# Kernel tuning notes

Measured on AMD Instinct MI355X. Metric: run time of the kernel, lower is better.

## Reference

```python
import math
import jax, jax.numpy as jnp
import numpy as np

B, T, D = 2, 2048, 1024
NUM_HEADS = 16
NUM_KV_HEADS = 4
HEAD_DIM = 64
ROPE_THETA = 500000.0


def precompute_freqs_cis(dim, seq_len, theta):
    freqs = 1.0 / theta ** (jnp.arange(0, dim, 2).astype(jnp.float32) / dim)
    freqs = jnp.outer(jnp.arange(seq_len), freqs)  # [T, dim//2]
    return jnp.cos(freqs), jnp.sin(freqs)


def apply_rotary_emb(xq, xk, cos, sin):
    # xq:[B,T,H,Dh], cos/sin:[T,Dh//2] -> broadcast as [1,T,1,Dh//2]
    c = cos[None, :, None, :]
    s = sin[None, :, None, :]

    def rot(x):
        xr = x.reshape(*x.shape[:-1], -1, 2)
        x0, x1 = xr[..., 0], xr[..., 1]
        return jnp.stack([x0 * c - x1 * s, x1 * c + x0 * s], axis=-1).reshape(x.shape)

    return rot(xq), rot(xk)


def setup_inputs() -> dict:
    key = jax.random.key(0)
    ks = jax.random.split(key, 5)
    x = jax.random.normal(ks[0], (B, T, D), dtype=jnp.float32)
    # causal mask [B,1,T,T]
    mask = jnp.broadcast_to(jnp.tril(jnp.ones((T, T), dtype=bool))[None, None], (B, 1, T, T))
    sq = 1.0 / math.sqrt(D)
    Wq = jax.random.normal(ks[1], (D, NUM_HEADS * HEAD_DIM), dtype=jnp.float32) * sq
    Wk = jax.random.normal(ks[2], (D, NUM_KV_HEADS * HEAD_DIM), dtype=jnp.float32) * sq
    Wv = jax.random.normal(ks[3], (D, NUM_KV_HEADS * HEAD_DIM), dtype=jnp.float32) * sq
    Wo = jax.random.normal(ks[4], (NUM_HEADS * HEAD_DIM, D), dtype=jnp.float32) * (1.0 / math.sqrt(NUM_HEADS * HEAD_DIM))
    return {"x": x, "mask": mask, "Wq": Wq, "Wk": Wk, "Wv": Wv, "Wo": Wo}


def reference(x, mask, Wq, Wk, Wv, Wo):
    b, t, _ = x.shape
    n_rep = NUM_HEADS // NUM_KV_HEADS
    q = (x @ Wq).reshape(b, t, NUM_HEADS, HEAD_DIM)
    k = (x @ Wk).reshape(b, t, NUM_KV_HEADS, HEAD_DIM)
    v = (x @ Wv).reshape(b, t, NUM_KV_HEADS, HEAD_DIM)
    cos, sin = precompute_freqs_cis(HEAD_DIM, t, ROPE_THETA)
    q, k = apply_rotary_emb(q, k, cos, sin)
    k = jnp.repeat(k, n_rep, axis=2)
    v = jnp.repeat(v, n_rep, axis=2)
    q = q.transpose(0, 2, 1, 3)  # [B,H,T,Dh]
    k = k.transpose(0, 2, 1, 3)
    v = v.transpose(0, 2, 1, 3)
    scale = 1.0 / math.sqrt(HEAD_DIM)
    attn = jnp.einsum('bhqd,bhkd->bhqk', q, k) * scale
    attn = jnp.where(mask, attn, -1e9)
    attn = jax.nn.softmax(attn, axis=-1)
    out = jnp.einsum('bhqk,bhkd->bhqd', attn, v)
    out = out.transpose(0, 2, 1, 3).reshape(b, t, -1)
    return out @ Wo
```

## Files before the change

### kernel.cpp

```cpp
#include <hip/hip_runtime.h>
#include <hip/hip_bf16.h>

#define B_  2
#define T_  2048
#define D_  1024
#define H_  16
#define KH_ 4
#define DH_ 64

typedef __attribute__((ext_vector_type(8))) short bf16x8;
typedef __attribute__((ext_vector_type(4))) float f32x4;

#define QSCALE 0.18033688011112043f

#if defined(__has_builtin)
#  if __has_builtin(__builtin_amdgcn_exp2f)
#    define EXP2F(x) __builtin_amdgcn_exp2f(x)
#  endif
#endif
#ifndef EXP2F
#  define EXP2F(x) exp2f(x)
#endif

__device__ __forceinline__ unsigned short f2bf(float f) {
  union { float f; unsigned int u; } v; v.f = f;
  return (unsigned short)((v.u + 0x7FFFu + ((v.u >> 16) & 1u)) >> 16);
}
__device__ __forceinline__ unsigned int pk2(float a, float b) {
  union { __hip_bfloat162 h2; unsigned int u; } v;
  v.h2 = __float22bfloat162_rn(make_float2(a, b));
  return v.u;
}

__device__ __forceinline__ void g2l16(const void* g, void* l) {
  __builtin_amdgcn_global_load_lds(
      (const __attribute__((address_space(1))) void*)g,
      (__attribute__((address_space(3))) void*)l, 16, 0, 0);
}


__global__ __launch_bounds__(256) void prep_kernel(
    const float* __restrict__ x,  const float* __restrict__ Wq,
    const float* __restrict__ Wk, const float* __restrict__ Wv,
    const float* __restrict__ Wo,
    short* __restrict__ xb, short* __restrict__ WT, short* __restrict__ WoT,
    float2* __restrict__ tbl) {
  __shared__ short Ts[64 * 72];
  const int bid = blockIdx.x, tid = threadIdx.x;

  if (bid < 2048) {
    const size_t i8 = ((size_t)bid * 256 + tid) * 8;
    const float4 a = *(const float4*)&x[i8];
    const float4 b = *(const float4*)&x[i8 + 4];
    uint4 p; p.x = pk2(a.x, a.y); p.y = pk2(a.z, a.w);
    p.z = pk2(b.x, b.y); p.w = pk2(b.z, b.w);
    *(uint4*)&xb[i8] = p;
  } else if (bid < 2688) {
    const bool isW = bid < 2432;
    const int idx = isW ? (bid - 2048) : (bid - 2432);
    const int n0 = (idx >> 4) * 64, k0 = (idx & 15) * 64;
    const float* src; int ncols, c0; short* dst;
    if (isW) {
      dst = WT;
      if (n0 < 1024)      { src = Wq; ncols = 1024; c0 = n0; }
      else if (n0 < 1280) { src = Wk; ncols = 256;  c0 = n0 - 1024; }
      else                { src = Wv; ncols = 256;  c0 = n0 - 1280; }
    } else { dst = WoT; src = Wo; ncols = 1024; c0 = n0; }
    for (int i = tid; i < 1024; i += 256) {
      const int kr = i >> 4, c4 = (i & 15) << 2;
      const int kc = isW ? kr : ((kr & 15) * 4 + (kr >> 4));
      const float4 w = *(const float4*)&src[(size_t)(k0 + kr) * ncols + c0 + c4];
      Ts[(c4 + 0) * 72 + kc] = (short)f2bf(w.x);
      Ts[(c4 + 1) * 72 + kc] = (short)f2bf(w.y);
      Ts[(c4 + 2) * 72 + kc] = (short)f2bf(w.z);
      Ts[(c4 + 3) * 72 + kc] = (short)f2bf(w.w);
    }
    __syncthreads();
    for (int c = tid; c < 512; c += 256) {
      const int nr = c >> 3, c8 = (c & 7) * 8;
      *(bf16x8*)&dst[(size_t)(n0 + nr) * 1024 + k0 + c8] =
          *(const bf16x8*)&Ts[nr * 72 + c8];
    }
  } else {
    const int e = (bid - 2688) * 256 + tid;
    const int t = e >> 5, i2 = e & 31;
    const float freq = exp2f(-(float)(2 * i2) * (18.931568569324174f / 64.0f));
    float sn, cs; sincosf((float)t * freq, &sn, &cs);
    tbl[e] = make_float2(cs, sn);
  }
}

__global__ __launch_bounds__(256) void qkv_mfma_kernel(
    const short* __restrict__ xb, const short* __restrict__ WT,
    const float2* __restrict__ tbl,
    short* __restrict__ qo, short* __restrict__ ko, short* __restrict__ vt) {
  __shared__ short Xs[128 * 128];
  __shared__ short Wt[64 * 128];
  const int tid = threadIdx.x;
  const int lane = tid & 63, w = tid >> 6;
  const int lm = lane & 15, quad = lane >> 4;
  const int lr = lane >> 4;
  const int lb = lane & 15;
  const int bid = blockIdx.x;
  const int xcd = bid & 7, slot = bid >> 3;
  const int mt = xcd * 4 + (slot & 3);
  const int nt = slot >> 2;
  const int m0 = mt * 128;
  const int n0 = nt * 64;

  f32x4 acc[2][4];
  #pragma unroll
  for (int sm = 0; sm < 2; ++sm)
    #pragma unroll
    for (int ct = 0; ct < 4; ++ct) acc[sm][ct] = (f32x4){0.f, 0.f, 0.f, 0.f};

  for (int kt = 0; kt < 8; ++kt) {
    __syncthreads();
    #pragma unroll
    for (int u = 0; u < 8; ++u) {
      const int r = (w * 8 + u) * 4 + lr;
      const int sb = lb ^ (r & 7);
      g2l16(&xb[(size_t)(m0 + r) * 1024 + kt * 128 + sb * 8],
            &Xs[(w * 8 + u) * 512]);
    }
    #pragma unroll
    for (int u = 0; u < 4; ++u) {
      const int r = (w * 4 + u) * 4 + lr;
      const int sb = lb ^ (r & 7);
      g2l16(&WT[(size_t)(n0 + r) * 1024 + kt * 128 + sb * 8],
            &Wt[(w * 4 + u) * 512]);
    }
    asm volatile("s_waitcnt vmcnt(0)" ::: "memory");
    __syncthreads();
    #pragma unroll
    for (int s = 0; s < 4; ++s) {
      bf16x8 bfr[4];
      #pragma unroll
      for (int ct = 0; ct < 4; ++ct)
        bfr[ct] = *(const bf16x8*)&Wt[(ct * 16 + lm) * 128 +
                                      (((s * 4 + quad) ^ (lm & 7)) << 3)];
      #pragma unroll
      for (int sm = 0; sm < 2; ++sm) {
        const bf16x8 a = *(const bf16x8*)&Xs[(w * 32 + sm * 16 + lm) * 128 +
                                             (((s * 4 + quad) ^ (lm & 7)) << 3)];
        #pragma unroll
        for (int ct = 0; ct < 4; ++ct)
          acc[sm][ct] =
              __builtin_amdgcn_mfma_f32_16x16x32_bf16(a, bfr[ct], acc[sm][ct], 0, 0, 0);
      }
    }
  }

  if (n0 < 1280) {
    const bool isQ = n0 < 1024;
    short* outp = isQ ? qo : ko;
    const int base = isQ ? n0 : n0 - 1024;
    const int nh = isQ ? H_ : KH_;
    const int hh = base >> 6;
    const float post = isQ ? QSCALE : 1.0f;
    #pragma unroll
    for (int sm = 0; sm < 2; ++sm)
      #pragma unroll
      for (int r = 0; r < 4; ++r) {
        const int row = m0 + w * 32 + sm * 16 + quad * 4 + r;
        const int b = row >> 11, t = row & 2047;
        float v4[4];
        #pragma unroll
        for (int ct = 0; ct < 4; ++ct) {
          float val = acc[sm][ct][r];
          const float other = __shfl_xor(val, 1);
          const int ci = ct * 16 + lm;
          const float2 cs = tbl[t * 32 + (ci >> 1)];
          val = ((ci & 1) == 0) ? (val * cs.x - other * cs.y)
                                : (val * cs.x + other * cs.y);
          v4[ct] = val * post;
        }
        uint2 st; st.x = pk2(v4[0], v4[1]); st.y = pk2(v4[2], v4[3]);
        *(uint2*)&outp[((size_t)(b * nh + hh) * T_ + t) * DH_ + lm * 4] = st;
      }
  } else {
    __syncthreads();
    #pragma unroll
    for (int sm = 0; sm < 2; ++sm)
      #pragma unroll
      for (int r = 0; r < 4; ++r)
        #pragma unroll
        for (int ct = 0; ct < 4; ++ct)
          Xs[(w * 32 + sm * 16 + quad * 4 + r) * 72 + ct * 16 + lm] =
              (short)f2bf(acc[sm][ct][r]);
    __syncthreads();
    const int kh = (n0 - 1280) >> 6;
    const int b = m0 >> 11, t0 = m0 & 2047;
    short* vb = vt + (size_t)(b * KH_ + kh) * DH_ * T_;
    for (int c = tid; c < 1024; c += 256) {
      const int d = c >> 4, c8 = (c & 15) * 8;
      short tmp[8];
      #pragma unroll
      for (int j = 0; j < 8; ++j) {
        const int s = c8 + j, sg = s & 63;
        const int tok = (s & 64) | (sg & 35) | (((sg >> 2) & 1) << 4) |
                        (((sg >> 3) & 3) << 2);
        tmp[j] = Xs[tok * 72 + d];
      }
      *(bf16x8*)&vb[(size_t)d * T_ + t0 + c8] = *(bf16x8*)tmp;
    }
  }
}

__global__ __launch_bounds__(256, 4) void attn_mfma_kernel(
    const short* __restrict__ q, const short* __restrict__ k,
    const short* __restrict__ vt, short* __restrict__ att) {
  __shared__ short Ks[128 * 72];
  __shared__ short Vts[64 * 136];

  const int bx = blockIdx.x;
  const int jj = bx & 255, c2 = bx >> 8;
  int qt = (c2 & 1) ? (jj >> 3) : (31 - (jj >> 3));
  const int hb = (jj & 7) | (c2 << 3);
  const int h = hb >> 1, b = hb & 1;
  const int kh = h >> 2;
  const int tid = threadIdx.x;
  const int lane = tid & 63, w = tid >> 6;
  const int lm = lane & 15, quad = lane >> 4;
  const int q0 = qt * 64;

  const short* qb = q + (size_t)(b * H_ + h) * T_ * DH_;
  const short* kb = k + (size_t)(b * KH_ + kh) * T_ * DH_;
  const short* vb = vt + (size_t)(b * KH_ + kh) * DH_ * T_;

  bf16x8 ones;
  #pragma unroll
  for (int i = 0; i < 8; ++i) ones[i] = (short)0x3F80;

  bf16x8 aq[2];
  #pragma unroll
  for (int s = 0; s < 2; ++s)
    aq[s] = *(const bf16x8*)&qb[(size_t)(q0 + w * 16 + lm) * 64 + s * 32 + quad * 8];

  bf16x8 pk[4], pv[4];
  #pragma unroll
  for (int u = 0; u < 4; ++u) {
    const int c = tid + u * 256;
    const int row = c >> 3, c8 = (c & 7) * 8;
    pk[u] = *(const bf16x8*)&kb[(size_t)row * 64 + c8];
    const int d = c >> 4, c16 = (c & 15) * 8;
    pv[u] = *(const bf16x8*)&vb[(size_t)d * T_ + c16];
  }

  f32x4 oacc[4], lacc;
  #pragma unroll
  for (int i = 0; i < 4; ++i) oacc[i] = (f32x4){0.f, 0.f, 0.f, 0.f};
  lacc = (f32x4){0.f, 0.f, 0.f, 0.f};

  auto step = [&](int j, bool diag) {
    f32x4 sacc[4];
    #pragma unroll
    for (int i = 0; i < 4; ++i) sacc[i] = (f32x4){0.f, 0.f, 0.f, 0.f};
    __builtin_amdgcn_s_setprio(1);
    #pragma unroll
    for (int s2 = 0; s2 < 2; ++s2) {
      #pragma unroll
      for (int ct = 0; ct < 4; ++ct) {
        if (diag && ct > w) continue;
        const bf16x8 bb =
            *(const bf16x8*)&Ks[(j * 64 + ct * 16 + lm) * 72 + s2 * 32 + quad * 8];
        sacc[ct] = __builtin_amdgcn_mfma_f32_16x16x32_bf16(bb, aq[s2], sacc[ct], 0, 0, 0);
      }
    }
    __builtin_amdgcn_s_setprio(0);
    unsigned int pd[4][2];
    #pragma unroll
    for (int ct = 0; ct < 4; ++ct) {
      float p[4];
      #pragma unroll
      for (int r = 0; r < 4; ++r) {
        float e;
        if (diag && ct > w) e = 0.f;
        else {
          e = EXP2F(sacc[ct][r]);
          if (diag && ct == w && (quad * 4 + r) > lm) e = 0.f;
        }
        p[r] = e;
      }
      pd[ct][0] = pk2(p[0], p[1]);
      pd[ct][1] = pk2(p[2], p[3]);
    }
    __builtin_amdgcn_s_setprio(1);
    #pragma unroll
    for (int s2 = 0; s2 < 2; ++s2) {
      if (diag && 2 * s2 > w) continue;
      union { bf16x8 v; unsigned int u[4]; } pa;
      pa.u[0] = pd[2 * s2][0];     pa.u[1] = pd[2 * s2][1];
      pa.u[2] = pd[2 * s2 + 1][0]; pa.u[3] = pd[2 * s2 + 1][1];
      lacc = __builtin_amdgcn_mfma_f32_16x16x32_bf16(pa.v, ones, lacc, 0, 0, 0);
      #pragma unroll
      for (int ct = 0; ct < 4; ++ct) {
        const bf16x8 vfr = *(const bf16x8*)&Vts[(ct * 16 + lm) * 136 +
                                                j * 64 + s2 * 32 + quad * 8];
        oacc[ct] = __builtin_amdgcn_mfma_f32_16x16x32_bf16(pa.v, vfr, oacc[ct], 0, 0, 0);
      }
    }
    __builtin_amdgcn_s_setprio(0);
  };

  auto stage = [&](int r2) {
    __syncthreads();
    #pragma unroll
    for (int u = 0; u < 4; ++u) {
      const int c = tid + u * 256;
      const int row = c >> 3, c8 = (c & 7) * 8;
      *(bf16x8*)&Ks[row * 72 + c8] = pk[u];
      const int d = c >> 4, c16 = (c & 15) * 8;
      *(bf16x8*)&Vts[d * 136 + c16] = pv[u];
    }
    __syncthreads();
    const int r2n = (r2 + 2 <= qt) ? (r2 + 2) : r2;
    #pragma unroll
    for (int u = 0; u < 4; ++u) {
      const int c = tid + u * 256;
      const int row = c >> 3, c8 = (c & 7) * 8;
      pk[u] = *(const bf16x8*)&kb[(size_t)(r2n * 64 + row) * 64 + c8];
      const int d = c >> 4, c16 = (c & 15) * 8;
      pv[u] = *(const bf16x8*)&vb[(size_t)d * T_ + r2n * 64 + c16];
    }
  };

  int r2 = 0;
  for (; r2 + 1 <= qt; r2 += 2) {
    stage(r2);
    step(0, false);
    step(1, r2 + 1 == qt);
  }
  if (r2 == qt) {
    stage(r2);
    step(0, true);
  }

  #pragma unroll
  for (int r = 0; r < 4; ++r) {
    const int qrow = q0 + w * 16 + quad * 4 + r;
    const float inv = 1.f / lacc[r];
    uint2 st;
    st.x = pk2(oacc[0][r] * inv, oacc[1][r] * inv);
    st.y = pk2(oacc[2][r] * inv, oacc[3][r] * inv);
    *(uint2*)&att[((size_t)b * T_ + qrow) * 1024 + h * 64 + lm * 4] = st;
  }
}

__global__ __launch_bounds__(256) void outproj_mfma_kernel(
    const short* __restrict__ att, const short* __restrict__ WoT,
    float* __restrict__ out) {
  __shared__ short Xs[128 * 128];
  __shared__ short Wt[64 * 128];
  const int tid = threadIdx.x;
  const int lane = tid & 63, w = tid >> 6;
  const int lm = lane & 15, quad = lane >> 4;
  const int lr = lane >> 4;
  const int lb = lane & 15;
  const int bid = blockIdx.x;
  const int xcd = bid & 7, slot = bid >> 3;
  const int m0 = (xcd * 4 + (slot & 3)) * 128;
  const int n0 = (slot >> 2) * 64;

  f32x4 acc[2][4];
  #pragma unroll
  for (int sm = 0; sm < 2; ++sm)
    #pragma unroll
    for (int ct = 0; ct < 4; ++ct) acc[sm][ct] = (f32x4){0.f, 0.f, 0.f, 0.f};

  for (int kt = 0; kt < 8; ++kt) {
    __syncthreads();
    #pragma unroll
    for (int u = 0; u < 8; ++u) {
      const int r = (w * 8 + u) * 4 + lr;
      const int sb = lb ^ (r & 7);
      g2l16(&att[(size_t)(m0 + r) * 1024 + kt * 128 + sb * 8],
            &Xs[(w * 8 + u) * 512]);
    }
    #pragma unroll
    for (int u = 0; u < 4; ++u) {
      const int r = (w * 4 + u) * 4 + lr;
      const int sb = lb ^ (r & 7);
      g2l16(&WoT[(size_t)(n0 + r) * 1024 + kt * 128 + sb * 8],
            &Wt[(w * 4 + u) * 512]);
    }
    asm volatile("s_waitcnt vmcnt(0)" ::: "memory");
    __syncthreads();
    #pragma unroll
    for (int s = 0; s < 4; ++s) {
      bf16x8 bfr[4];
      #pragma unroll
      for (int ct = 0; ct < 4; ++ct)
        bfr[ct] = *(const bf16x8*)&Wt[(ct * 16 + lm) * 128 +
                                      (((s * 4 + quad) ^ (lm & 7)) << 3)];
      #pragma unroll
      for (int sm = 0; sm < 2; ++sm) {
        const bf16x8 a = *(const bf16x8*)&Xs[(w * 32 + sm * 16 + lm) * 128 +
                                             (((s * 4 + quad) ^ (lm & 7)) << 3)];
        #pragma unroll
        for (int ct = 0; ct < 4; ++ct)
          acc[sm][ct] =
              __builtin_amdgcn_mfma_f32_16x16x32_bf16(a, bfr[ct], acc[sm][ct], 0, 0, 0);
      }
    }
  }

  #pragma unroll
  for (int sm = 0; sm < 2; ++sm)
    #pragma unroll
    for (int r = 0; r < 4; ++r) {
      const int row = m0 + w * 32 + sm * 16 + quad * 4 + r;
      #pragma unroll
      for (int ct = 0; ct < 4; ++ct)
        out[(size_t)row * 1024 + n0 + ct * 16 + lm] = acc[sm][ct][r];
    }
}

extern "C" void kernel_launch(void* const* d_in, const int* in_sizes, int n_in,
                              void* d_out, int out_size, void* d_ws, size_t ws_size,
                              hipStream_t stream) {
  const float* x  = (const float*)d_in[0];
  const float* Wq = (const float*)d_in[2];
  const float* Wk = (const float*)d_in[3];
  const float* Wv = (const float*)d_in[4];
  const float* Wo = (const float*)d_in[5];
  float* out = (float*)d_out;

  short* xb   = (short*)d_ws;
  short* WT   = xb  + (size_t)4194304;
  short* WoT  = WT  + (size_t)1572864;
  short* qb   = WoT + (size_t)1048576;
  short* kb   = qb  + (size_t)4194304;
  short* vtb  = kb  + (size_t)1048576;
  short* attb = vtb + (size_t)1048576;
  float2* tbl = (float2*)(attb + (size_t)4194304);

  prep_kernel<<<dim3(2944), dim3(256), 0, stream>>>(
      x, Wq, Wk, Wv, Wo, xb, WT, WoT, tbl);
  qkv_mfma_kernel<<<dim3(768), dim3(256), 0, stream>>>(xb, WT, tbl, qb, kb, vtb);
  attn_mfma_kernel<<<dim3(1024), dim3(256), 0, stream>>>(qb, kb, vtb, attb);
  outproj_mfma_kernel<<<dim3(512), dim3(256), 0, stream>>>(attb, WoT, out);
}
```

Before: 169.0 us.

## Process two query heads sharing a KV head per attention block

```diff
diff --git a/kernel.cpp b/kernel.cpp
--- a/kernel.cpp
+++ b/kernel.cpp
@@ -207,7 +207,7 @@
   }
 }
 
-__global__ __launch_bounds__(256, 4) void attn_mfma_kernel(
+__global__ __launch_bounds__(256, 2) void attn_mfma_kernel(
     const short* __restrict__ q, const short* __restrict__ k,
     const short* __restrict__ vt, short* __restrict__ att) {
   __shared__ short Ks[128 * 72];
@@ -217,14 +217,16 @@
   const int jj = bx & 255, c2 = bx >> 8;
   int qt = (c2 & 1) ? (jj >> 3) : (31 - (jj >> 3));
   const int hb = (jj & 7) | (c2 << 3);
-  const int h = hb >> 1, b = hb & 1;
-  const int kh = h >> 2;
+  const int hp = hb >> 1, b = hb & 1;
+  const int h0 = hp * 2, h1 = h0 + 1;
+  const int kh = h0 >> 2;
   const int tid = threadIdx.x;
   const int lane = tid & 63, w = tid >> 6;
   const int lm = lane & 15, quad = lane >> 4;
   const int q0 = qt * 64;
 
-  const short* qb = q + (size_t)(b * H_ + h) * T_ * DH_;
+  const short* qb0 = q + (size_t)(b * H_ + h0) * T_ * DH_;
+  const short* qb1 = qb0 + (size_t)T_ * DH_;
   const short* kb = k + (size_t)(b * KH_ + kh) * T_ * DH_;
   const short* vb = vt + (size_t)(b * KH_ + kh) * DH_ * T_;
 
@@ -232,10 +234,13 @@
   #pragma unroll
   for (int i = 0; i < 8; ++i) ones[i] = (short)0x3F80;
 
-  bf16x8 aq[2];
-  #pragma unroll
-  for (int s = 0; s < 2; ++s)
-    aq[s] = *(const bf16x8*)&qb[(size_t)(q0 + w * 16 + lm) * 64 + s * 32 + quad * 8];
+  bf16x8 aq0[2], aq1[2];
+  #pragma unroll
+  for (int s = 0; s < 2; ++s) {
+    const size_t off = (size_t)(q0 + w * 16 + lm) * 64 + s * 32 + quad * 8;
+    aq0[s] = *(const bf16x8*)&qb0[off];
+    aq1[s] = *(const bf16x8*)&qb1[off];
+  }
 
   bf16x8 pk[4], pv[4];
   #pragma unroll
@@ -247,15 +252,22 @@
     pv[u] = *(const bf16x8*)&vb[(size_t)d * T_ + c16];
   }
 
-  f32x4 oacc[4], lacc;
-  #pragma unroll
-  for (int i = 0; i < 4; ++i) oacc[i] = (f32x4){0.f, 0.f, 0.f, 0.f};
-  lacc = (f32x4){0.f, 0.f, 0.f, 0.f};
+  f32x4 oacc0[4], oacc1[4], lacc0, lacc1;
+  #pragma unroll
+  for (int i = 0; i < 4; ++i) {
+    oacc0[i] = (f32x4){0.f, 0.f, 0.f, 0.f};
+    oacc1[i] = (f32x4){0.f, 0.f, 0.f, 0.f};
+  }
+  lacc0 = (f32x4){0.f, 0.f, 0.f, 0.f};
+  lacc1 = (f32x4){0.f, 0.f, 0.f, 0.f};
 
   auto step = [&](int j, bool diag) {
-    f32x4 sacc[4];
-    #pragma unroll
-    for (int i = 0; i < 4; ++i) sacc[i] = (f32x4){0.f, 0.f, 0.f, 0.f};
+    f32x4 sacc0[4], sacc1[4];
+    #pragma unroll
+    for (int i = 0; i < 4; ++i) {
+      sacc0[i] = (f32x4){0.f, 0.f, 0.f, 0.f};
+      sacc1[i] = (f32x4){0.f, 0.f, 0.f, 0.f};
+    }
     __builtin_amdgcn_s_setprio(1);
     #pragma unroll
     for (int s2 = 0; s2 < 2; ++s2) {
@@ -264,40 +276,46 @@
         if (diag && ct > w) continue;
         const bf16x8 bb =
             *(const bf16x8*)&Ks[(j * 64 + ct * 16 + lm) * 72 + s2 * 32 + quad * 8];
-        sacc[ct] = __builtin_amdgcn_mfma_f32_16x16x32_bf16(bb, aq[s2], sacc[ct], 0, 0, 0);
+        sacc0[ct] = __builtin_amdgcn_mfma_f32_16x16x32_bf16(bb, aq0[s2], sacc0[ct], 0, 0, 0);
+        sacc1[ct] = __builtin_amdgcn_mfma_f32_16x16x32_bf16(bb, aq1[s2], sacc1[ct], 0, 0, 0);
       }
     }
     __builtin_amdgcn_s_setprio(0);
-    unsigned int pd[4][2];
+    unsigned int pd0[4][2], pd1[4][2];
     #pragma unroll
     for (int ct = 0; ct < 4; ++ct) {
-      float p[4];
+      float p0[4], p1[4];
       #pragma unroll
       for (int r = 0; r < 4; ++r) {
-        float e;
-        if (diag && ct > w) e = 0.f;
+        float e0, e1;
+        if (diag && ct > w) { e0 = 0.f; e1 = 0.f; }
         else {
-          e = EXP2F(sacc[ct][r]);
-          if (diag && ct == w && (quad * 4 + r) > lm) e = 0.f;
+          e0 = EXP2F(sacc0[ct][r]);
+          e1 = EXP2F(sacc1[ct][r]);
+          if (diag && ct == w && (quad * 4 + r) > lm) { e0 = 0.f; e1 = 0.f; }
         }
-        p[r] = e;
-      }
-      pd[ct][0] = pk2(p[0], p[1]);
-      pd[ct][1] = pk2(p[2], p[3]);
+        p0[r] = e0; p1[r] = e1;
+      }
+      pd0[ct][0] = pk2(p0[0], p0[1]); pd0[ct][1] = pk2(p0[2], p0[3]);
+      pd1[ct][0] = pk2(p1[0], p1[1]); pd1[ct][1] = pk2(p1[2], p1[3]);
     }
     __builtin_amdgcn_s_setprio(1);
     #pragma unroll
     for (int s2 = 0; s2 < 2; ++s2) {
       if (diag && 2 * s2 > w) continue;
-      union { bf16x8 v; unsigned int u[4]; } pa;
-      pa.u[0] = pd[2 * s2][0];     pa.u[1] = pd[2 * s2][1];
-      pa.u[2] = pd[2 * s2 + 1][0]; pa.u[3] = pd[2 * s2 + 1][1];
-      lacc = __builtin_amdgcn_mfma_f32_16x16x32_bf16(pa.v, ones, lacc, 0, 0, 0);
+      union { bf16x8 v; unsigned int u[4]; } pa0, pa1;
+      pa0.u[0] = pd0[2 * s2][0];     pa0.u[1] = pd0[2 * s2][1];
+      pa0.u[2] = pd0[2 * s2 + 1][0]; pa0.u[3] = pd0[2 * s2 + 1][1];
+      pa1.u[0] = pd1[2 * s2][0];     pa1.u[1] = pd1[2 * s2][1];
+      pa1.u[2] = pd1[2 * s2 + 1][0]; pa1.u[3] = pd1[2 * s2 + 1][1];
+      lacc0 = __builtin_amdgcn_mfma_f32_16x16x32_bf16(pa0.v, ones, lacc0, 0, 0, 0);
+      lacc1 = __builtin_amdgcn_mfma_f32_16x16x32_bf16(pa1.v, ones, lacc1, 0, 0, 0);
       #pragma unroll
       for (int ct = 0; ct < 4; ++ct) {
         const bf16x8 vfr = *(const bf16x8*)&Vts[(ct * 16 + lm) * 136 +
                                                 j * 64 + s2 * 32 + quad * 8];
-        oacc[ct] = __builtin_amdgcn_mfma_f32_16x16x32_bf16(pa.v, vfr, oacc[ct], 0, 0, 0);
+        oacc0[ct] = __builtin_amdgcn_mfma_f32_16x16x32_bf16(pa0.v, vfr, oacc0[ct], 0, 0, 0);
+        oacc1[ct] = __builtin_amdgcn_mfma_f32_16x16x32_bf16(pa1.v, vfr, oacc1[ct], 0, 0, 0);
       }
     }
     __builtin_amdgcn_s_setprio(0);
@@ -339,11 +357,15 @@
   #pragma unroll
   for (int r = 0; r < 4; ++r) {
     const int qrow = q0 + w * 16 + quad * 4 + r;
-    const float inv = 1.f / lacc[r];
+    const float inv0 = 1.f / lacc0[r];
     uint2 st;
-    st.x = pk2(oacc[0][r] * inv, oacc[1][r] * inv);
-    st.y = pk2(oacc[2][r] * inv, oacc[3][r] * inv);
-    *(uint2*)&att[((size_t)b * T_ + qrow) * 1024 + h * 64 + lm * 4] = st;
+    st.x = pk2(oacc0[0][r] * inv0, oacc0[1][r] * inv0);
+    st.y = pk2(oacc0[2][r] * inv0, oacc0[3][r] * inv0);
+    *(uint2*)&att[((size_t)b * T_ + qrow) * 1024 + h0 * 64 + lm * 4] = st;
+    const float inv1 = 1.f / lacc1[r];
+    st.x = pk2(oacc1[0][r] * inv1, oacc1[1][r] * inv1);
+    st.y = pk2(oacc1[2][r] * inv1, oacc1[3][r] * inv1);
+    *(uint2*)&att[((size_t)b * T_ + qrow) * 1024 + h1 * 64 + lm * 4] = st;
   }
 }
 
@@ -438,6 +460,6 @@
   prep_kernel<<<dim3(2944), dim3(256), 0, stream>>>(
       x, Wq, Wk, Wv, Wo, xb, WT, WoT, tbl);
   qkv_mfma_kernel<<<dim3(768), dim3(256), 0, stream>>>(xb, WT, tbl, qb, kb, vtb);
-  attn_mfma_kernel<<<dim3(1024), dim3(256), 0, stream>>>(qb, kb, vtb, attb);
+  attn_mfma_kernel<<<dim3(512), dim3(256), 0, stream>>>(qb, kb, vtb, attb);
   outproj_mfma_kernel<<<dim3(512), dim3(256), 0, stream>>>(attb, WoT, out);
 }
```

Measured after the change: 179.0 us. 5.9% more time.

## Double-buffer GEMM K-tiles and fuse paired attention steps

Applied to the files above, without the earlier changes.

```diff
diff --git a/kernel.cpp b/kernel.cpp
--- a/kernel.cpp
+++ b/kernel.cpp
@@ -94,19 +94,15 @@
     const short* __restrict__ xb, const short* __restrict__ WT,
     const float2* __restrict__ tbl,
     short* __restrict__ qo, short* __restrict__ ko, short* __restrict__ vt) {
-  __shared__ short Xs[128 * 128];
-  __shared__ short Wt[64 * 128];
+  __shared__ short Xsh[2][128 * 64];
+  __shared__ short Wth[2][64 * 64];
   const int tid = threadIdx.x;
   const int lane = tid & 63, w = tid >> 6;
   const int lm = lane & 15, quad = lane >> 4;
-  const int lr = lane >> 4;
-  const int lb = lane & 15;
   const int bid = blockIdx.x;
   const int xcd = bid & 7, slot = bid >> 3;
-  const int mt = xcd * 4 + (slot & 3);
-  const int nt = slot >> 2;
-  const int m0 = mt * 128;
-  const int n0 = nt * 64;
+  const int m0 = (xcd * 4 + (slot & 3)) * 128;
+  const int n0 = (slot >> 2) * 64;
 
   f32x4 acc[2][4];
   #pragma unroll
@@ -114,41 +110,53 @@
     #pragma unroll
     for (int ct = 0; ct < 4; ++ct) acc[sm][ct] = (f32x4){0.f, 0.f, 0.f, 0.f};
 
-  for (int kt = 0; kt < 8; ++kt) {
-    __syncthreads();
-    #pragma unroll
-    for (int u = 0; u < 8; ++u) {
-      const int r = (w * 8 + u) * 4 + lr;
-      const int sb = lb ^ (r & 7);
-      g2l16(&xb[(size_t)(m0 + r) * 1024 + kt * 128 + sb * 8],
-            &Xs[(w * 8 + u) * 512]);
-    }
+  auto stage = [&](int kt, int bsel) {
     #pragma unroll
     for (int u = 0; u < 4; ++u) {
-      const int r = (w * 4 + u) * 4 + lr;
-      const int sb = lb ^ (r & 7);
-      g2l16(&WT[(size_t)(n0 + r) * 1024 + kt * 128 + sb * 8],
-            &Wt[(w * 4 + u) * 512]);
-    }
-    asm volatile("s_waitcnt vmcnt(0)" ::: "memory");
-    __syncthreads();
-    #pragma unroll
-    for (int s = 0; s < 4; ++s) {
+      const int r = u * 32 + w * 8 + (lane >> 3);
+      const int sb = (lane & 7) ^ (r & 7);
+      g2l16(&xb[(size_t)(m0 + r) * 1024 + kt * 64 + sb * 8],
+            &Xsh[bsel][(u * 32 + w * 8) * 64]);
+    }
+    #pragma unroll
+    for (int u = 0; u < 2; ++u) {
+      const int r = u * 32 + w * 8 + (lane >> 3);
+      const int sb = (lane & 7) ^ (r & 7);
+      g2l16(&WT[(size_t)(n0 + r) * 1024 + kt * 64 + sb * 8],
+            &Wth[bsel][(u * 32 + w * 8) * 64]);
+    }
+  };
+
+  stage(0, 0);
+  for (int kt = 0; kt < 16; ++kt) {
+    const int bsel = kt & 1;
+    if (kt < 15) {
+      stage(kt + 1, bsel ^ 1);
+      asm volatile("s_waitcnt vmcnt(6)" ::: "memory");
+    } else {
+      asm volatile("s_waitcnt vmcnt(0)" ::: "memory");
+    }
+    __builtin_amdgcn_s_barrier();
+    __builtin_amdgcn_sched_barrier(0);
+    #pragma unroll
+    for (int s2 = 0; s2 < 2; ++s2) {
       bf16x8 bfr[4];
       #pragma unroll
       for (int ct = 0; ct < 4; ++ct)
-        bfr[ct] = *(const bf16x8*)&Wt[(ct * 16 + lm) * 128 +
-                                      (((s * 4 + quad) ^ (lm & 7)) << 3)];
+        bfr[ct] = *(const bf16x8*)&Wth[bsel][(ct * 16 + lm) * 64 +
+                                            (((s2 * 4 + quad) ^ (lm & 7)) << 3)];
       #pragma unroll
       for (int sm = 0; sm < 2; ++sm) {
-        const bf16x8 a = *(const bf16x8*)&Xs[(w * 32 + sm * 16 + lm) * 128 +
-                                             (((s * 4 + quad) ^ (lm & 7)) << 3)];
+        const bf16x8 a = *(const bf16x8*)&Xsh[bsel][(w * 32 + sm * 16 + lm) * 64 +
+                                            (((s2 * 4 + quad) ^ (lm & 7)) << 3)];
         #pragma unroll
         for (int ct = 0; ct < 4; ++ct)
           acc[sm][ct] =
               __builtin_amdgcn_mfma_f32_16x16x32_bf16(a, bfr[ct], acc[sm][ct], 0, 0, 0);
       }
     }
+    __builtin_amdgcn_sched_barrier(0);
+    __builtin_amdgcn_s_barrier();
   }
 
   if (n0 < 1280) {
@@ -179,6 +187,7 @@
         *(uint2*)&outp[((size_t)(b * nh + hh) * T_ + t) * DH_ + lm * 4] = st;
       }
   } else {
+    short* XsF = &Xsh[0][0];
     __syncthreads();
     #pragma unroll
     for (int sm = 0; sm < 2; ++sm)
@@ -186,7 +195,7 @@
       for (int r = 0; r < 4; ++r)
         #pragma unroll
         for (int ct = 0; ct < 4; ++ct)
-          Xs[(w * 32 + sm * 16 + quad * 4 + r) * 72 + ct * 16 + lm] =
+          XsF[(w * 32 + sm * 16 + quad * 4 + r) * 72 + ct * 16 + lm] =
               (short)f2bf(acc[sm][ct][r]);
     __syncthreads();
     const int kh = (n0 - 1280) >> 6;
@@ -200,7 +209,7 @@
         const int s = c8 + j, sg = s & 63;
         const int tok = (s & 64) | (sg & 35) | (((sg >> 2) & 1) << 4) |
                         (((sg >> 3) & 3) << 2);
-        tmp[j] = Xs[tok * 72 + d];
+        tmp[j] = XsF[tok * 72 + d];
       }
       *(bf16x8*)&vb[(size_t)d * T_ + t0 + c8] = *(bf16x8*)tmp;
     }
@@ -252,21 +261,103 @@
   for (int i = 0; i < 4; ++i) oacc[i] = (f32x4){0.f, 0.f, 0.f, 0.f};
   lacc = (f32x4){0.f, 0.f, 0.f, 0.f};
 
-  auto step = [&](int j, bool diag) {
+  auto pairstep = [&](bool diag1) {
+    f32x4 sacc0[4], sacc1[4];
+    #pragma unroll
+    for (int i = 0; i < 4; ++i) {
+      sacc0[i] = (f32x4){0.f, 0.f, 0.f, 0.f};
+      sacc1[i] = (f32x4){0.f, 0.f, 0.f, 0.f};
+    }
+    __builtin_amdgcn_s_setprio(1);
+    #pragma unroll
+    for (int s2 = 0; s2 < 2; ++s2)
+      #pragma unroll
+      for (int ct = 0; ct < 4; ++ct) {
+        const bf16x8 bb =
+            *(const bf16x8*)&Ks[(ct * 16 + lm) * 72 + s2 * 32 + quad * 8];
+        sacc0[ct] = __builtin_amdgcn_mfma_f32_16x16x32_bf16(bb, aq[s2], sacc0[ct], 0, 0, 0);
+      }
+    #pragma unroll
+    for (int s2 = 0; s2 < 2; ++s2)
+      #pragma unroll
+      for (int ct = 0; ct < 4; ++ct) {
+        if (diag1 && ct > w) continue;
+        const bf16x8 bb =
+            *(const bf16x8*)&Ks[(64 + ct * 16 + lm) * 72 + s2 * 32 + quad * 8];
+        sacc1[ct] = __builtin_amdgcn_mfma_f32_16x16x32_bf16(bb, aq[s2], sacc1[ct], 0, 0, 0);
+      }
+    __builtin_amdgcn_s_setprio(0);
+    unsigned int pd0[4][2];
+    #pragma unroll
+    for (int ct = 0; ct < 4; ++ct) {
+      float p[4];
+      #pragma unroll
+      for (int r = 0; r < 4; ++r) p[r] = EXP2F(sacc0[ct][r]);
+      pd0[ct][0] = pk2(p[0], p[1]); pd0[ct][1] = pk2(p[2], p[3]);
+    }
+    __builtin_amdgcn_s_setprio(1);
+    #pragma unroll
+    for (int s2 = 0; s2 < 2; ++s2) {
+      union { bf16x8 v; unsigned int u[4]; } pa;
+      pa.u[0] = pd0[2 * s2][0];     pa.u[1] = pd0[2 * s2][1];
+      pa.u[2] = pd0[2 * s2 + 1][0]; pa.u[3] = pd0[2 * s2 + 1][1];
+      lacc = __builtin_amdgcn_mfma_f32_16x16x32_bf16(pa.v, ones, lacc, 0, 0, 0);
+      #pragma unroll
+      for (int ct = 0; ct < 4; ++ct) {
+        const bf16x8 vfr = *(const bf16x8*)&Vts[(ct * 16 + lm) * 136 +
+                                                s2 * 32 + quad * 8];
+        oacc[ct] = __builtin_amdgcn_mfma_f32_16x16x32_bf16(pa.v, vfr, oacc[ct], 0, 0, 0);
+      }
+    }
+    __builtin_amdgcn_s_setprio(0);
+    unsigned int pd1[4][2];
+    #pragma unroll
+    for (int ct = 0; ct < 4; ++ct) {
+      float p[4];
+      #pragma unroll
+      for (int r = 0; r < 4; ++r) {
+        float e;
+        if (diag1 && ct > w) e = 0.f;
+        else {
+          e = EXP2F(sacc1[ct][r]);
+          if (diag1 && ct == w && (quad * 4 + r) > lm) e = 0.f;
+        }
+        p[r] = e;
+      }
+      pd1[ct][0] = pk2(p[0], p[1]); pd1[ct][1] = pk2(p[2], p[3]);
+    }
+    __builtin_amdgcn_s_setprio(1);
+    #pragma unroll
+    for (int s2 = 0; s2 < 2; ++s2) {
+      if (diag1 && 2 * s2 > w) continue;
+      union { bf16x8 v; unsigned int u[4]; } pa;
+      pa.u[0] = pd1[2 * s2][0];     pa.u[1] = pd1[2 * s2][1];
+      pa.u[2] = pd1[2 * s2 + 1][0]; pa.u[3] = pd1[2 * s2 + 1][1];
+      lacc = __builtin_amdgcn_mfma_f32_16x16x32_bf16(pa.v, ones, lacc, 0, 0, 0);
+      #pragma unroll
+      for (int ct = 0; ct < 4; ++ct) {
+        const bf16x8 vfr = *(const bf16x8*)&Vts[(ct * 16 + lm) * 136 +
+                                                64 + s2 * 32 + quad * 8];
+        oacc[ct] = __builtin_amdgcn_mfma_f32_16x16x32_bf16(pa.v, vfr, oacc[ct], 0, 0, 0);
+      }
+    }
+    __builtin_amdgcn_s_setprio(0);
+  };
+
+  auto dstep = [&]() {
     f32x4 sacc[4];
     #pragma unroll
     for (int i = 0; i < 4; ++i) sacc[i] = (f32x4){0.f, 0.f, 0.f, 0.f};
     __builtin_amdgcn_s_setprio(1);
     #pragma unroll
-    for (int s2 = 0; s2 < 2; ++s2) {
+    for (int s2 = 0; s2 < 2; ++s2)
       #pragma unroll
       for (int ct = 0; ct < 4; ++ct) {
-        if (diag && ct > w) continue;
+        if (ct > w) continue;
         const bf16x8 bb =
-            *(const bf16x8*)&Ks[(j * 64 + ct * 16 + lm) * 72 + s2 * 32 + quad * 8];
+            *(const bf16x8*)&Ks[(ct * 16 + lm) * 72 + s2 * 32 + quad * 8];
         sacc[ct] = __builtin_amdgcn_mfma_f32_16x16x32_bf16(bb, aq[s2], sacc[ct], 0, 0, 0);
       }
-    }
     __builtin_amdgcn_s_setprio(0);
     unsigned int pd[4][2];
     #pragma unroll
@@ -275,20 +366,19 @@
       #pragma unroll
       for (int r = 0; r < 4; ++r) {
         float e;
-        if (diag && ct > w) e = 0.f;
+        if (ct > w) e = 0.f;
         else {
           e = EXP2F(sacc[ct][r]);
-          if (diag && ct == w && (quad * 4 + r) > lm) e = 0.f;
+          if (ct == w && (quad * 4 + r) > lm) e = 0.f;
         }
         p[r] = e;
       }
-      pd[ct][0] = pk2(p[0], p[1]);
-      pd[ct][1] = pk2(p[2], p[3]);
+      pd[ct][0] = pk2(p[0], p[1]); pd[ct][1] = pk2(p[2], p[3]);
     }
     __builtin_amdgcn_s_setprio(1);
     #pragma unroll
     for (int s2 = 0; s2 < 2; ++s2) {
-      if (diag && 2 * s2 > w) continue;
+      if (2 * s2 > w) continue;
       union { bf16x8 v; unsigned int u[4]; } pa;
       pa.u[0] = pd[2 * s2][0];     pa.u[1] = pd[2 * s2][1];
       pa.u[2] = pd[2 * s2 + 1][0]; pa.u[3] = pd[2 * s2 + 1][1];
@@ -296,7 +386,7 @@
       #pragma unroll
       for (int ct = 0; ct < 4; ++ct) {
         const bf16x8 vfr = *(const bf16x8*)&Vts[(ct * 16 + lm) * 136 +
-                                                j * 64 + s2 * 32 + quad * 8];
+                                                s2 * 32 + quad * 8];
         oacc[ct] = __builtin_amdgcn_mfma_f32_16x16x32_bf16(pa.v, vfr, oacc[ct], 0, 0, 0);
       }
     }
@@ -328,12 +418,11 @@
   int r2 = 0;
   for (; r2 + 1 <= qt; r2 += 2) {
     stage(r2);
-    step(0, false);
-    step(1, r2 + 1 == qt);
+    pairstep(r2 + 1 == qt);
   }
   if (r2 == qt) {
     stage(r2);
-    step(0, true);
+    dstep();
   }
 
   #pragma unroll
@@ -350,13 +439,11 @@
 __global__ __launch_bounds__(256) void outproj_mfma_kernel(
     const short* __restrict__ att, const short* __restrict__ WoT,
     float* __restrict__ out) {
-  __shared__ short Xs[128 * 128];
-  __shared__ short Wt[64 * 128];
+  __shared__ short Xsh[2][128 * 64];
+  __shared__ short Wth[2][64 * 64];
   const int tid = threadIdx.x;
   const int lane = tid & 63, w = tid >> 6;
   const int lm = lane & 15, quad = lane >> 4;
-  const int lr = lane >> 4;
-  const int lb = lane & 15;
   const int bid = blockIdx.x;
   const int xcd = bid & 7, slot = bid >> 3;
   const int m0 = (xcd * 4 + (slot & 3)) * 128;
@@ -368,41 +455,53 @@
     #pragma unroll
     for (int ct = 0; ct < 4; ++ct) acc[sm][ct] = (f32x4){0.f, 0.f, 0.f, 0.f};
 
-  for (int kt = 0; kt < 8; ++kt) {
-    __syncthreads();
-    #pragma unroll
-    for (int u = 0; u < 8; ++u) {
-      const int r = (w * 8 + u) * 4 + lr;
-      const int sb = lb ^ (r & 7);
-      g2l16(&att[(size_t)(m0 + r) * 1024 + kt * 128 + sb * 8],
-            &Xs[(w * 8 + u) * 512]);
-    }
+  auto stage = [&](int kt, int bsel) {
     #pragma unroll
     for (int u = 0; u < 4; ++u) {
-      const int r = (w * 4 + u) * 4 + lr;
-      const int sb = lb ^ (r & 7);
-      g2l16(&WoT[(size_t)(n0 + r) * 1024 + kt * 128 + sb * 8],
-            &Wt[(w * 4 + u) * 512]);
-    }
-    asm volatile("s_waitcnt vmcnt(0)" ::: "memory");
-    __syncthreads();
-    #pragma unroll
-    for (int s = 0; s < 4; ++s) {
+      const int r = u * 32 + w * 8 + (lane >> 3);
+      const int sb = (lane & 7) ^ (r & 7);
+      g2l16(&att[(size_t)(m0 + r) * 1024 + kt * 64 + sb * 8],
+            &Xsh[bsel][(u * 32 + w * 8) * 64]);
+    }
+    #pragma unroll
+    for (int u = 0; u < 2; ++u) {
+      const int r = u * 32 + w * 8 + (lane >> 3);
+      const int sb = (lane & 7) ^ (r & 7);
+      g2l16(&WoT[(size_t)(n0 + r) * 1024 + kt * 64 + sb * 8],
+            &Wth[bsel][(u * 32 + w * 8) * 64]);
+    }
+  };
+
+  stage(0, 0);
+  for (int kt = 0; kt < 16; ++kt) {
+    const int bsel = kt & 1;
+    if (kt < 15) {
+      stage(kt + 1, bsel ^ 1);
+      asm volatile("s_waitcnt vmcnt(6)" ::: "memory");
+    } else {
+      asm volatile("s_waitcnt vmcnt(0)" ::: "memory");
+    }
+    __builtin_amdgcn_s_barrier();
+    __builtin_amdgcn_sched_barrier(0);
+    #pragma unroll
+    for (int s2 = 0; s2 < 2; ++s2) {
       bf16x8 bfr[4];
       #pragma unroll
       for (int ct = 0; ct < 4; ++ct)
-        bfr[ct] = *(const bf16x8*)&Wt[(ct * 16 + lm) * 128 +
-                                      (((s * 4 + quad) ^ (lm & 7)) << 3)];
+        bfr[ct] = *(const bf16x8*)&Wth[bsel][(ct * 16 + lm) * 64 +
+                                            (((s2 * 4 + quad) ^ (lm & 7)) << 3)];
       #pragma unroll
       for (int sm = 0; sm < 2; ++sm) {
-        const bf16x8 a = *(const bf16x8*)&Xs[(w * 32 + sm * 16 + lm) * 128 +
-                                             (((s * 4 + quad) ^ (lm & 7)) << 3)];
+        const bf16x8 a = *(const bf16x8*)&Xsh[bsel][(w * 32 + sm * 16 + lm) * 64 +
+                                            (((s2 * 4 + quad) ^ (lm & 7)) << 3)];
         #pragma unroll
         for (int ct = 0; ct < 4; ++ct)
           acc[sm][ct] =
               __builtin_amdgcn_mfma_f32_16x16x32_bf16(a, bfr[ct], acc[sm][ct], 0, 0, 0);
       }
     }
+    __builtin_amdgcn_sched_barrier(0);
+    __builtin_amdgcn_s_barrier();
   }
 
   #pragma unroll
```

Result: no change. 168.9 us (median of 2 runs) (-0.1%).

## Double-buffer GEMM k-loop and enlarge tiles to 128x128 with 2x2 warp grid

Applied to the files above, without the earlier changes.

```diff
diff --git a/kernel.cpp b/kernel.cpp
--- a/kernel.cpp
+++ b/kernel.cpp
@@ -94,75 +94,85 @@
     const short* __restrict__ xb, const short* __restrict__ WT,
     const float2* __restrict__ tbl,
     short* __restrict__ qo, short* __restrict__ ko, short* __restrict__ vt) {
-  __shared__ short Xs[128 * 128];
-  __shared__ short Wt[64 * 128];
+  __shared__ short SB[2 * 16384];
   const int tid = threadIdx.x;
   const int lane = tid & 63, w = tid >> 6;
   const int lm = lane & 15, quad = lane >> 4;
-  const int lr = lane >> 4;
-  const int lb = lane & 15;
+  const int wm = w >> 1, wn = w & 1;
   const int bid = blockIdx.x;
   const int xcd = bid & 7, slot = bid >> 3;
-  const int mt = xcd * 4 + (slot & 3);
-  const int nt = slot >> 2;
-  const int m0 = mt * 128;
-  const int n0 = nt * 64;
-
-  f32x4 acc[2][4];
-  #pragma unroll
-  for (int sm = 0; sm < 2; ++sm)
+  const int m0 = (xcd * 4 + (slot & 3)) * 128;
+  const int n0 = (slot >> 2) * 128;
+
+  f32x4 acc[4][4];
+  #pragma unroll
+  for (int sm = 0; sm < 4; ++sm)
     #pragma unroll
     for (int ct = 0; ct < 4; ++ct) acc[sm][ct] = (f32x4){0.f, 0.f, 0.f, 0.f};
 
-  for (int kt = 0; kt < 8; ++kt) {
-    __syncthreads();
-    #pragma unroll
-    for (int u = 0; u < 8; ++u) {
-      const int r = (w * 8 + u) * 4 + lr;
-      const int sb = lb ^ (r & 7);
-      g2l16(&xb[(size_t)(m0 + r) * 1024 + kt * 128 + sb * 8],
-            &Xs[(w * 8 + u) * 512]);
-    }
-    #pragma unroll
-    for (int u = 0; u < 4; ++u) {
-      const int r = (w * 4 + u) * 4 + lr;
-      const int sb = lb ^ (r & 7);
-      g2l16(&WT[(size_t)(n0 + r) * 1024 + kt * 128 + sb * 8],
-            &Wt[(w * 4 + u) * 512]);
-    }
-    asm volatile("s_waitcnt vmcnt(0)" ::: "memory");
-    __syncthreads();
-    #pragma unroll
-    for (int s = 0; s < 4; ++s) {
-      bf16x8 bfr[4];
+  auto stage = [&](int kt, int bsel) {
+    #pragma unroll
+    for (int u = 0; u < 4; ++u) {
+      const int r = u * 32 + w * 8 + (lane >> 3);
+      const int sb = (lane & 7) ^ (r & 7);
+      g2l16(&xb[(size_t)(m0 + r) * 1024 + kt * 64 + sb * 8],
+            &SB[bsel * 16384 + (u * 32 + w * 8) * 64]);
+    }
+    #pragma unroll
+    for (int u = 0; u < 4; ++u) {
+      const int r = u * 32 + w * 8 + (lane >> 3);
+      const int sb = (lane & 7) ^ (r & 7);
+      g2l16(&WT[(size_t)(n0 + r) * 1024 + kt * 64 + sb * 8],
+            &SB[bsel * 16384 + 8192 + (u * 32 + w * 8) * 64]);
+    }
+  };
+
+  stage(0, 0);
+  for (int kt = 0; kt < 16; ++kt) {
+    const int bsel = kt & 1;
+    if (kt < 15) {
+      stage(kt + 1, bsel ^ 1);
+      asm volatile("s_waitcnt vmcnt(8)" ::: "memory");
+    } else {
+      asm volatile("s_waitcnt vmcnt(0)" ::: "memory");
+    }
+    __builtin_amdgcn_s_barrier();
+    __builtin_amdgcn_sched_barrier(0);
+    #pragma unroll
+    for (int s2 = 0; s2 < 2; ++s2) {
+      const int ko = ((s2 * 4 + quad) ^ (lm & 7)) << 3;
+      bf16x8 bfr[4], afr[4];
       #pragma unroll
       for (int ct = 0; ct < 4; ++ct)
-        bfr[ct] = *(const bf16x8*)&Wt[(ct * 16 + lm) * 128 +
-                                      (((s * 4 + quad) ^ (lm & 7)) << 3)];
-      #pragma unroll
-      for (int sm = 0; sm < 2; ++sm) {
-        const bf16x8 a = *(const bf16x8*)&Xs[(w * 32 + sm * 16 + lm) * 128 +
-                                             (((s * 4 + quad) ^ (lm & 7)) << 3)];
+        bfr[ct] = *(const bf16x8*)&SB[bsel * 16384 + 8192 +
+                                      (wn * 64 + ct * 16 + lm) * 64 + ko];
+      #pragma unroll
+      for (int sm = 0; sm < 4; ++sm)
+        afr[sm] = *(const bf16x8*)&SB[bsel * 16384 +
+                                      (wm * 64 + sm * 16 + lm) * 64 + ko];
+      #pragma unroll
+      for (int sm = 0; sm < 4; ++sm)
         #pragma unroll
         for (int ct = 0; ct < 4; ++ct)
           acc[sm][ct] =
-              __builtin_amdgcn_mfma_f32_16x16x32_bf16(a, bfr[ct], acc[sm][ct], 0, 0, 0);
-      }
-    }
+              __builtin_amdgcn_mfma_f32_16x16x32_bf16(afr[sm], bfr[ct], acc[sm][ct], 0, 0, 0);
+    }
+    __builtin_amdgcn_sched_barrier(0);
+    __builtin_amdgcn_s_barrier();
   }
 
   if (n0 < 1280) {
     const bool isQ = n0 < 1024;
     short* outp = isQ ? qo : ko;
-    const int base = isQ ? n0 : n0 - 1024;
+    const int nbase = n0 + wn * 64 - (isQ ? 0 : 1024);
     const int nh = isQ ? H_ : KH_;
-    const int hh = base >> 6;
+    const int hh = nbase >> 6;
     const float post = isQ ? QSCALE : 1.0f;
     #pragma unroll
-    for (int sm = 0; sm < 2; ++sm)
+    for (int sm = 0; sm < 4; ++sm)
       #pragma unroll
       for (int r = 0; r < 4; ++r) {
-        const int row = m0 + w * 32 + sm * 16 + quad * 4 + r;
+        const int row = m0 + wm * 64 + sm * 16 + quad * 4 + r;
         const int b = row >> 11, t = row & 2047;
         float v4[4];
         #pragma unroll
@@ -179,28 +189,31 @@
         *(uint2*)&outp[((size_t)(b * nh + hh) * T_ + t) * DH_ + lm * 4] = st;
       }
   } else {
+    const int khbase = (n0 - 1280) >> 6;
     __syncthreads();
     #pragma unroll
-    for (int sm = 0; sm < 2; ++sm)
+    for (int sm = 0; sm < 4; ++sm)
       #pragma unroll
       for (int r = 0; r < 4; ++r)
         #pragma unroll
-        for (int ct = 0; ct < 4; ++ct)
-          Xs[(w * 32 + sm * 16 + quad * 4 + r) * 72 + ct * 16 + lm] =
+        for (int ct = 0; ct < 4; ++ct) {
+          const int tok = wm * 64 + sm * 16 + quad * 4 + r;
+          SB[wn * 9216 + tok * 72 + ct * 16 + lm] =
               (short)f2bf(acc[sm][ct][r]);
+        }
     __syncthreads();
-    const int kh = (n0 - 1280) >> 6;
     const int b = m0 >> 11, t0 = m0 & 2047;
-    short* vb = vt + (size_t)(b * KH_ + kh) * DH_ * T_;
-    for (int c = tid; c < 1024; c += 256) {
-      const int d = c >> 4, c8 = (c & 15) * 8;
+    for (int c = tid; c < 2048; c += 256) {
+      const int hw = c >> 10, cc = c & 1023;
+      const int d = cc >> 4, c8 = (cc & 15) * 8;
+      short* vb = vt + (size_t)(b * KH_ + khbase + hw) * DH_ * T_;
       short tmp[8];
       #pragma unroll
       for (int j = 0; j < 8; ++j) {
         const int s = c8 + j, sg = s & 63;
         const int tok = (s & 64) | (sg & 35) | (((sg >> 2) & 1) << 4) |
                         (((sg >> 3) & 3) << 2);
-        tmp[j] = Xs[tok * 72 + d];
+        tmp[j] = SB[hw * 9216 + tok * 72 + d];
       }
       *(bf16x8*)&vb[(size_t)d * T_ + t0 + c8] = *(bf16x8*)tmp;
     }
@@ -350,69 +363,81 @@
 __global__ __launch_bounds__(256) void outproj_mfma_kernel(
     const short* __restrict__ att, const short* __restrict__ WoT,
     float* __restrict__ out) {
-  __shared__ short Xs[128 * 128];
-  __shared__ short Wt[64 * 128];
+  __shared__ short SB[2 * 16384];
   const int tid = threadIdx.x;
   const int lane = tid & 63, w = tid >> 6;
   const int lm = lane & 15, quad = lane >> 4;
-  const int lr = lane >> 4;
-  const int lb = lane & 15;
+  const int wm = w >> 1, wn = w & 1;
   const int bid = blockIdx.x;
   const int xcd = bid & 7, slot = bid >> 3;
   const int m0 = (xcd * 4 + (slot & 3)) * 128;
-  const int n0 = (slot >> 2) * 64;
-
-  f32x4 acc[2][4];
-  #pragma unroll
-  for (int sm = 0; sm < 2; ++sm)
+  const int n0 = (slot >> 2) * 128;
+
+  f32x4 acc[4][4];
+  #pragma unroll
+  for (int sm = 0; sm < 4; ++sm)
     #pragma unroll
     for (int ct = 0; ct < 4; ++ct) acc[sm][ct] = (f32x4){0.f, 0.f, 0.f, 0.f};
 
-  for (int kt = 0; kt < 8; ++kt) {
-    __syncthreads();
-    #pragma unroll
-    for (int u = 0; u < 8; ++u) {
-      const int r = (w * 8 + u) * 4 + lr;
-      const int sb = lb ^ (r & 7);
-      g2l16(&att[(size_t)(m0 + r) * 1024 + kt * 128 + sb * 8],
-            &Xs[(w * 8 + u) * 512]);
-    }
-    #pragma unroll
-    for (int u = 0; u < 4; ++u) {
-      const int r = (w * 4 + u) * 4 + lr;
-      const int sb = lb ^ (r & 7);
-      g2l16(&WoT[(size_t)(n0 + r) * 1024 + kt * 128 + sb * 8],
-            &Wt[(w * 4 + u) * 512]);
-    }
-    asm volatile("s_waitcnt vmcnt(0)" ::: "memory");
-    __syncthreads();
-    #pragma unroll
-    for (int s = 0; s < 4; ++s) {
-      bf16x8 bfr[4];
+  auto stage = [&](int kt, int bsel) {
+    #pragma unroll
+    for (int u = 0; u < 4; ++u) {
+      const int r = u * 32 + w * 8 + (lane >> 3);
+      const int sb = (lane & 7) ^ (r & 7);
+      g2l16(&att[(size_t)(m0 + r) * 1024 + kt * 64 + sb * 8],
+            &SB[bsel * 16384 + (u * 32 + w * 8) * 64]);
+    }
+    #pragma unroll
+    for (int u = 0; u < 4; ++u) {
+      const int r = u * 32 + w * 8 + (lane >> 3);
+      const int sb = (lane & 7) ^ (r & 7);
+      g2l16(&WoT[(size_t)(n0 + r) * 1024 + kt * 64 + sb * 8],
+            &SB[bsel * 16384 + 8192 + (u * 32 + w * 8) * 64]);
+    }
+  };
+
+  stage(0, 0);
+  for (int kt = 0; kt < 16; ++kt) {
+    const int bsel = kt & 1;
+    if (kt < 15) {
+      stage(kt + 1, bsel ^ 1);
+      asm volatile("s_waitcnt vmcnt(8)" ::: "memory");
+    } else {
+      asm volatile("s_waitcnt vmcnt(0)" ::: "memory");
+    }
+    __builtin_amdgcn_s_barrier();
+    __builtin_amdgcn_sched_barrier(0);
+    #pragma unroll
+    for (int s2 = 0; s2 < 2; ++s2) {
+      const int ko = ((s2 * 4 + quad) ^ (lm & 7)) << 3;
+      bf16x8 bfr[4], afr[4];
       #pragma unroll
       for (int ct = 0; ct < 4; ++ct)
-        bfr[ct] = *(const bf16x8*)&Wt[(ct * 16 + lm) * 128 +
-                                      (((s * 4 + quad) ^ (lm & 7)) << 3)];
-      #pragma unroll
-      for (int sm = 0; sm < 2; ++sm) {
-        const bf16x8 a = *(const bf16x8*)&Xs[(w * 32 + sm * 16 + lm) * 128 +
-                                             (((s * 4 + quad) ^ (lm & 7)) << 3)];
+        bfr[ct] = *(const bf16x8*)&SB[bsel * 16384 + 8192 +
+                                      (wn * 64 + ct * 16 + lm) * 64 + ko];
+      #pragma unroll
+      for (int sm = 0; sm < 4; ++sm)
+        afr[sm] = *(const bf16x8*)&SB[bsel * 16384 +
+                                      (wm * 64 + sm * 16 + lm) * 64 + ko];
+      #pragma unroll
+      for (int sm = 0; sm < 4; ++sm)
         #pragma unroll
         for (int ct = 0; ct < 4; ++ct)
           acc[sm][ct] =
-              __builtin_amdgcn_mfma_f32_16x16x32_bf16(a, bfr[ct], acc[sm][ct], 0, 0, 0);
-      }
-    }
-  }
-
-  #pragma unroll
-  for (int sm = 0; sm < 2; ++sm)
+              __builtin_amdgcn_mfma_f32_16x16x32_bf16(afr[sm], bfr[ct], acc[sm][ct], 0, 0, 0);
+    }
+    __builtin_amdgcn_sched_barrier(0);
+    __builtin_amdgcn_s_barrier();
+  }
+
+  #pragma unroll
+  for (int sm = 0; sm < 4; ++sm)
     #pragma unroll
     for (int r = 0; r < 4; ++r) {
-      const int row = m0 + w * 32 + sm * 16 + quad * 4 + r;
+      const int row = m0 + wm * 64 + sm * 16 + quad * 4 + r;
       #pragma unroll
       for (int ct = 0; ct < 4; ++ct)
-        out[(size_t)row * 1024 + n0 + ct * 16 + lm] = acc[sm][ct][r];
+        out[(size_t)row * 1024 + n0 + wn * 64 + ct * 16 + lm] = acc[sm][ct][r];
     }
 }
 
@@ -437,7 +462,7 @@
 
   prep_kernel<<<dim3(2944), dim3(256), 0, stream>>>(
       x, Wq, Wk, Wv, Wo, xb, WT, WoT, tbl);
-  qkv_mfma_kernel<<<dim3(768), dim3(256), 0, stream>>>(xb, WT, tbl, qb, kb, vtb);
+  qkv_mfma_kernel<<<dim3(384), dim3(256), 0, stream>>>(xb, WT, tbl, qb, kb, vtb);
   attn_mfma_kernel<<<dim3(1024), dim3(256), 0, stream>>>(qb, kb, vtb, attb);
-  outproj_mfma_kernel<<<dim3(512), dim3(256), 0, stream>>>(attb, WoT, out);
-}
+  outproj_mfma_kernel<<<dim3(256), dim3(256), 0, stream>>>(attb, WoT, out);
+}
```

Measured after the change: 171.4 us. About the same (+1.4%).
